# Performance work log

Measured on AMD Instinct MI355X. Metric: run time of the kernel, lower is better.

## Reference

```python
import jax, jax.numpy as jnp
import numpy as np

K = 16
REP = 128
ASZ = 6
AENC = 64
BSK = 2048 * K  # bs*K flat batch


def _lin(k, fin, fout):
    return jax.random.normal(k, (fin, fout), jnp.float32) / np.float32(np.sqrt(fin))


def setup_inputs() -> dict:
    key = jax.random.key(0)
    ks = jax.random.split(key, 20)
    inp = {
        "lambda1": jax.random.normal(ks[0], (BSK, REP), jnp.float32),
        "actions": jax.random.normal(ks[1], (BSK, ASZ), jnp.float32),
    }
    # (fan_in, hidden, fan_out) per rlkit Mlp((hidden,), out, in)
    specs = {
        "le": (REP, REP, REP),            # lambda_encoder
        "ae": (ASZ, REP, AENC),           # action_encoder
        "aef": (AENC + REP, REP, REP),    # action_effect_network
        "aat": (AENC + REP, REP, 1),      # action_attention_network
        "pe": (2 * REP, 2 * REP, REP),    # pairwise_encoder_network
        "ie": (REP, REP, AENC),           # interaction_effect_network
        "ia": (REP, REP, 1),              # interaction_attention_network
        "fm": (AENC + REP, REP, REP),     # final_merge_network
    }
    i = 2
    for name, (fin, h, fout) in specs.items():
        inp[name + "_W1"] = _lin(ks[i], fin, h)
        inp[name + "_b1"] = jnp.zeros((h,), jnp.float32)
        inp[name + "_W2"] = _lin(ks[i + 1], h, fout)
        inp[name + "_b2"] = jnp.zeros((fout,), jnp.float32)
        i += 2
    return inp


def _mlp(x, W1, b1, W2, b2, out_act):
    h = jax.nn.elu(x @ W1 + b1)
    return out_act(h @ W2 + b2)


# constant all-pairs index lists (i != j), i-major as in the torch loop
_II = np.array([i for i in range(K) for j in range(K) if i != j])
_JJ = np.array([j for i in range(K) for j in range(K) if i != j])


def reference(lambda1, actions,
              le_W1, le_b1, le_W2, le_b2,
              ae_W1, ae_b1, ae_W2, ae_b2,
              aef_W1, aef_b1, aef_W2, aef_b2,
              aat_W1, aat_b1, aat_W2, aat_b2,
              pe_W1, pe_b1, pe_W2, pe_b2,
              ie_W1, ie_b1, ie_W2, ie_b2,
              ia_W1, ia_b1, ia_W2, ia_b2,
              fm_W1, fm_b1, fm_W2, fm_b2):
    elu, sig = jax.nn.elu, jax.nn.sigmoid
    ident = lambda z: z

    enc_flat = _mlp(lambda1, le_W1, le_b1, le_W2, le_b2, elu)        # (BSK, REP)
    a_enc = _mlp(actions, ae_W1, ae_b1, ae_W2, ae_b2, elu)           # (BSK, AENC)
    la = jnp.concatenate([enc_flat, a_enc], -1)                      # (BSK, REP+AENC)
    a_eff = _mlp(la, aef_W1, aef_b1, aef_W2, aef_b2, elu)            # (BSK, REP)
    a_att = _mlp(la, aat_W1, aat_b1, aat_W2, aat_b2, sig)            # (BSK, 1)
    enc = (a_eff * a_att).reshape(-1, K, REP)                        # (bs, K, REP)
    bs = enc.shape[0]

    # all ordered pairs (i, j), i != j -> concat sender/receiver states
    all_pairs = jnp.concatenate([enc[:, _II], enc[:, _JJ]], -1)      # (bs, K*(K-1), 2*REP)
    all_pairs = all_pairs.reshape(bs * K, K - 1, 2 * REP)

    pi = _mlp(all_pairs, pe_W1, pe_b1, pe_W2, pe_b2, elu)            # (bs*K, K-1, REP)
    effect = _mlp(pi, ie_W1, ie_b1, ie_W2, ie_b2, elu)               # (bs*K, K-1, AENC)
    attention = _mlp(pi, ia_W1, ia_b1, ia_W2, ia_b2, sig)            # (bs*K, K-1, 1)
    total_effect = (effect * attention).sum(1)                       # (bs*K, AENC)

    lam_eff = jnp.concatenate([enc_flat, total_effect], -1)          # (bs*K, REP+AENC)
    new_lambdas = _mlp(lam_eff, fm_W1, fm_b1, fm_W2, fm_b2, ident)   # (bs*K, REP)
    return new_lambdas
```

## Files before the change

### kernel.cpp

```cpp
#include <hip/hip_runtime.h>
#include <hip/hip_bf16.h>

typedef unsigned short ushort_t;
typedef unsigned int uint_t;
typedef short bf16x8 __attribute__((ext_vector_type(8)));
typedef float f32x4 __attribute__((ext_vector_type(4)));

#define MFMA16(a, b, c) __builtin_amdgcn_mfma_f32_16x16x32_bf16((a), (b), (c), 0, 0, 0)

__device__ __forceinline__ ushort_t f2bf(float f) {
  uint_t u = __float_as_uint(f);
  u += 0x7fffu + ((u >> 16) & 1u);
  return (ushort_t)(u >> 16);
}
__device__ __forceinline__ float bf2f(ushort_t h) {
  return __uint_as_float(((uint_t)h) << 16);
}
__device__ __forceinline__ uint_t pack2(float lo, float hi) {
  union { __hip_bfloat162 h; uint_t u; } cv;
  cv.h = __float22bfloat162_rn(float2{lo, hi});
  return cv.u;
}
__device__ __forceinline__ uint2 pack4(f32x4 v) {
  uint2 o;
  o.x = pack2(v[0], v[1]);
  o.y = pack2(v[2], v[3]);
  return o;
}
__device__ __forceinline__ float eluf(float x) {
  float e = __expf(x) - 1.0f;
  return x > 0.0f ? x : e;
}
__device__ __forceinline__ float sigmf(float x) {
  return 1.0f / (1.0f + __expf(-x));
}
__device__ __forceinline__ int lds_off(int row, int colb, int ccb) {
  return row * ccb + (colb ^ ((row & 7) << 4));
}

constexpr size_t OFF_ENCF = 0;
constexpr size_t OFF_ENC  = 4194304;
constexpr size_t OFF_TEFF = 8388608;
constexpr size_t OFF_FR   = 10485760;

constexpr int FR_LE_W1  = 0;
constexpr int FR_LE_W2  = 16384;
constexpr int FR_AE_W2  = 32768;
constexpr int FR_AEF_W1 = 40960;
constexpr int FR_AAT_W1 = 65536;
constexpr int FR_AEF_W2 = 90112;
constexpr int FR_PE_W1  = 106496;
constexpr int FR_PE_W2  = 172032;
constexpr int FR_IE_W1  = 204800;
constexpr int FR_IE_W2  = 221184;
constexpr int FR_IA_W1  = 229376;
constexpr int FR_FM_W1  = 245760;
constexpr int FR_FM_W2  = 270336;

struct PrepDesc { const float* src; ushort_t* dst; int K; int N; };
struct PrepArgs { PrepDesc d[13]; };

__global__ __launch_bounds__(256) void prep_kernel(PrepArgs a) {
  PrepDesc p = a.d[blockIdx.y];
  int idx = blockIdx.x * 256 + threadIdx.x;
  if (idx >= p.K * p.N) return;
  int e = idx & 7;
  int lane = (idx >> 3) & 63;
  int f = idx >> 9;
  int ksteps = p.K >> 5;
  int kstep = f % ksteps;
  int ntile = f / ksteps;
  int k = kstep * 32 + ((lane >> 4) << 3) + e;
  int n = ntile * 16 + (lane & 15);
  p.dst[idx] = f2bf(p.src[k * p.N + n]);
}


template <int MT, int NT, int KS>
__device__ __forceinline__ void reg_gemm_t(const bf16x8 x[MT][KS],
                                           const ushort_t* __restrict__ wfrag,
                                           int ntile0, int lane, f32x4 acc[MT][NT]) {
  const f32x4 z = {0.f, 0.f, 0.f, 0.f};
#pragma unroll
  for (int nt = 0; nt < NT; ++nt) {
#pragma unroll
    for (int m = 0; m < MT; ++m) acc[m][nt] = z;
    const ushort_t* wf = wfrag + (size_t)((ntile0 + nt) * KS) * 512 + lane * 8;
#pragma unroll
    for (int ks = 0; ks < KS; ++ks) {
      bf16x8 wfr = *(const bf16x8*)(wf + ks * 512);
#pragma unroll
      for (int m = 0; m < MT; ++m) acc[m][nt] = MFMA16(wfr, x[m][ks], acc[m][nt]);
    }
  }
}

template <int MT, int NT, int KS>
__device__ __forceinline__ void lds_gemm_t(const ushort_t* __restrict__ Abase,
                                           const ushort_t* __restrict__ wfrag,
                                           int ntile0, int lane, f32x4 acc[MT][NT]) {
  const int r = lane & 15, q = lane >> 4;
  bf16x8 x[MT][KS];
#pragma unroll
  for (int m = 0; m < MT; ++m)
#pragma unroll
    for (int ks = 0; ks < KS; ++ks) {
      int row = m * 16 + r;
      x[m][ks] = *(const bf16x8*)((const char*)Abase + lds_off(row, ks * 64 + q * 16, KS * 64));
    }
  reg_gemm_t<MT, NT, KS>(x, wfrag, ntile0, lane, acc);
}

template <int MT, int NT, bool ELU>
__device__ __forceinline__ void add_bias_act_t(f32x4 acc[MT][NT], const float* __restrict__ bias,
                                               int col0, int lane) {
  const int q = lane >> 4;
#pragma unroll
  for (int nt = 0; nt < NT; ++nt) {
    f32x4 bv = *(const f32x4*)(bias + col0 + nt * 16 + q * 4);
#pragma unroll
    for (int m = 0; m < MT; ++m)
#pragma unroll
      for (int k = 0; k < 4; ++k) {
        float v = acc[m][nt][k] + bv[k];
        acc[m][nt][k] = ELU ? eluf(v) : v;
      }
  }
}

template <int MT, int NT, int CCB>
__device__ __forceinline__ void store_lds_t(ushort_t* Dbase, int col0, int lane,
                                            const f32x4 acc[MT][NT]) {
  const int r = lane & 15, q = lane >> 4;
#pragma unroll
  for (int m = 0; m < MT; ++m) {
    const int row = m * 16 + r;
#pragma unroll
    for (int nt = 0; nt < NT; ++nt) {
      int colb = (col0 + nt * 16 + q * 4) * 2;
      *(uint2*)((char*)Dbase + lds_off(row, colb, CCB)) = pack4(acc[m][nt]);
    }
  }
}

template <int MT, int NT>
__device__ __forceinline__ void store_global_t(ushort_t* __restrict__ G, int row0, int ncols,
                                               int col0, int lane, const f32x4 acc[MT][NT]) {
  const int r = lane & 15, q = lane >> 4;
#pragma unroll
  for (int m = 0; m < MT; ++m)
#pragma unroll
    for (int nt = 0; nt < NT; ++nt)
      *(uint2*)(G + (size_t)(row0 + m * 16 + r) * ncols + col0 + nt * 16 + q * 4) =
          pack4(acc[m][nt]);
}

__global__ __launch_bounds__(256, 2) void enc_kernel(
    const float* __restrict__ lambda1, const float* __restrict__ actions,
    const float* __restrict__ le_b1, const float* __restrict__ le_b2,
    const float* __restrict__ ae_W1, const float* __restrict__ ae_b1,
    const float* __restrict__ ae_b2, const float* __restrict__ aef_b1,
    const float* __restrict__ aef_b2, const float* __restrict__ aat_b1,
    const float* __restrict__ aat_W2, const float* __restrict__ aat_b2,
    const ushort_t* __restrict__ fr, ushort_t* __restrict__ encf, ushort_t* __restrict__ enc) {
  __shared__ ushort_t bufA[64 * 128];
  __shared__ ushort_t bufB[64 * 128];
  __shared__ ushort_t la[64 * 192];
  __shared__ float att[64];

  const int t = threadIdx.x, lane = t & 63, w = t >> 6;
  const int r = lane & 15, q = lane >> 4;
  const int rows0 = blockIdx.x * 64;

  {
    const int row = t >> 2, c0 = (t & 3) * 32;
    const float4* src = (const float4*)(lambda1 + (size_t)(rows0 + row) * 128 + c0);
#pragma unroll
    for (int j = 0; j < 8; ++j) {
      float4 v = src[j];
      f32x4 vv = {v.x, v.y, v.z, v.w};
      *(uint2*)((char*)bufA + lds_off(row, (c0 + j * 4) * 2, 256)) = pack4(vv);
    }
  }
  __syncthreads();

  f32x4 acc2[4][2];
  lds_gemm_t<4, 2, 4>(bufA, fr + FR_LE_W1, w * 2, lane, acc2);
  add_bias_act_t<4, 2, true>(acc2, le_b1, w * 32, lane);
  store_lds_t<4, 2, 256>(bufB, w * 32, lane, acc2);
  __syncthreads();
  lds_gemm_t<4, 2, 4>(bufB, fr + FR_LE_W2, w * 2, lane, acc2);
  add_bias_act_t<4, 2, true>(acc2, le_b2, w * 32, lane);
  store_lds_t<4, 2, 384>(la, w * 32, lane, acc2);
  store_global_t<4, 2>(encf, rows0, 128, w * 32, lane, acc2);
  {
    const int row = t >> 2, c0 = (t & 3) * 32;
    float a6[6];
#pragma unroll
    for (int k2 = 0; k2 < 6; ++k2) a6[k2] = actions[(size_t)(rows0 + row) * 6 + k2];
#pragma unroll
    for (int j = 0; j < 16; ++j) {
      int c = c0 + j * 2;
      float s0 = ae_b1[c], s1 = ae_b1[c + 1];
#pragma unroll
      for (int k2 = 0; k2 < 6; ++k2) {
        s0 += a6[k2] * ae_W1[k2 * 128 + c];
        s1 += a6[k2] * ae_W1[k2 * 128 + c + 1];
      }
      *(uint_t*)((char*)bufA + lds_off(row, c * 2, 256)) = pack2(eluf(s0), eluf(s1));
    }
  }
  __syncthreads();
  {
    f32x4 acc1[4][1];
    lds_gemm_t<4, 1, 4>(bufA, fr + FR_AE_W2, w, lane, acc1);
    add_bias_act_t<4, 1, true>(acc1, ae_b2, w * 16, lane);
    store_lds_t<4, 1, 384>(la, 128 + w * 16, lane, acc1);
  }
  __syncthreads();
  lds_gemm_t<4, 2, 6>(la, fr + FR_AEF_W1, w * 2, lane, acc2);
  add_bias_act_t<4, 2, true>(acc2, aef_b1, w * 32, lane);
  store_lds_t<4, 2, 256>(bufA, w * 32, lane, acc2);
  lds_gemm_t<4, 2, 6>(la, fr + FR_AAT_W1, w * 2, lane, acc2);
  add_bias_act_t<4, 2, true>(acc2, aat_b1, w * 32, lane);
  store_lds_t<4, 2, 256>(bufB, w * 32, lane, acc2);
  __syncthreads();
  lds_gemm_t<4, 2, 4>(bufA, fr + FR_AEF_W2, w * 2, lane, acc2);
  add_bias_act_t<4, 2, true>(acc2, aef_b2, w * 32, lane);
  {
    const int row = t >> 2, s = t & 3;
    float sum = 0.f;
#pragma unroll
    for (int j = 0; j < 32; ++j) {
      int c = s * 32 + j;
      sum += bf2f(*(const ushort_t*)((const char*)bufB + lds_off(row, c * 2, 256))) * aat_W2[c];
    }
    sum += __shfl_xor(sum, 1);
    sum += __shfl_xor(sum, 2);
    if (s == 0) att[row] = sigmf(sum + aat_b2[0]);
  }
  __syncthreads();
#pragma unroll
  for (int mt = 0; mt < 4; ++mt) {
    float av = att[mt * 16 + r];
#pragma unroll
    for (int nt = 0; nt < 2; ++nt) {
      f32x4 sv = acc2[mt][nt];
      sv[0] *= av; sv[1] *= av; sv[2] *= av; sv[3] *= av;
      *(uint2*)(enc + (size_t)(rows0 + mt * 16 + r) * 128 + w * 32 + nt * 16 + q * 4) = pack4(sv);
    }
  }
}

__global__ __launch_bounds__(256, 3) void pair_kernel(
    const ushort_t* __restrict__ enc, const ushort_t* __restrict__ fr,
    const float* __restrict__ pe_b1, const float* __restrict__ pe_b2,
    const float* __restrict__ ie_b1, const float* __restrict__ ie_b2,
    const float* __restrict__ ia_b1, const float* __restrict__ ia_W2,
    const float* __restrict__ ia_b2, ushort_t* __restrict__ teff) {
  __shared__ ushort_t bufH[32 * 256];
  __shared__ ushort_t bufPi[32 * 128];
  __shared__ float att[32];

  const int t = threadIdx.x, lane = t & 63, w = t >> 6;
  const int r = lane & 15, q = lane >> 4;
  const int g0 = blockIdx.x * 2;
  const int b = g0 >> 4;

  bf16x8 x[2][8];
#pragma unroll
  for (int mt = 0; mt < 2; ++mt) {
    const int im = (g0 + mt) & 15;
#pragma unroll
    for (int ks = 0; ks < 8; ++ks) {
      const int srow = (ks < 4) ? im : r;
      const int k = (ks & 3) * 32 + q * 8;
      x[mt][ks] = *(const bf16x8*)(enc + (size_t)(b * 16 + srow) * 128 + k);
    }
  }
  {
    f32x4 acc[2][4];
    reg_gemm_t<2, 4, 8>(x, fr + FR_PE_W1, w * 4, lane, acc);
    add_bias_act_t<2, 4, true>(acc, pe_b1, w * 64, lane);
    store_lds_t<2, 4, 512>(bufH, w * 64, lane, acc);
  }
  __syncthreads();
  {
    f32x4 acc[2][2];
    lds_gemm_t<2, 2, 8>(bufH, fr + FR_PE_W2, w * 2, lane, acc);
    add_bias_act_t<2, 2, true>(acc, pe_b2, w * 32, lane);
    store_lds_t<2, 2, 256>(bufPi, w * 32, lane, acc);
  }
  __syncthreads();
  {
    f32x4 acc[2][2];
    lds_gemm_t<2, 2, 4>(bufPi, fr + FR_IE_W1, w * 2, lane, acc);
    add_bias_act_t<2, 2, true>(acc, ie_b1, w * 32, lane);
    store_lds_t<2, 2, 256>(bufH, w * 32, lane, acc);
    lds_gemm_t<2, 2, 4>(bufPi, fr + FR_IA_W1, w * 2, lane, acc);
    add_bias_act_t<2, 2, true>(acc, ia_b1, w * 32, lane);
    store_lds_t<2, 2, 256>(bufH + 32 * 128, w * 32, lane, acc);
  }
  __syncthreads();
  f32x4 eff[2][1];
  lds_gemm_t<2, 1, 4>(bufH, fr + FR_IE_W2, w, lane, eff);
  add_bias_act_t<2, 1, true>(eff, ie_b2, w * 16, lane);
  {
    const int row = t >> 3, s = t & 7;
    const char* hia = (const char*)(bufH + 32 * 128);
    float sum = 0.f;
#pragma unroll
    for (int j = 0; j < 16; ++j) {
      int c = s * 16 + j;
      sum += bf2f(*(const ushort_t*)(hia + lds_off(row, c * 2, 256))) * ia_W2[c];
    }
    sum += __shfl_xor(sum, 1);
    sum += __shfl_xor(sum, 2);
    sum += __shfl_xor(sum, 4);
    if (s == 0) att[row] = sigmf(sum + ia_b2[0]);
  }
  __syncthreads();
#pragma unroll
  for (int mt = 0; mt < 2; ++mt) {
    const int im = (g0 + mt) & 15;
    const float av = (r == im) ? 0.f : att[mt * 16 + r];
    float v0 = eff[mt][0][0] * av, v1 = eff[mt][0][1] * av;
    float v2 = eff[mt][0][2] * av, v3 = eff[mt][0][3] * av;
#pragma unroll
    for (int d = 1; d < 16; d <<= 1) {
      v0 += __shfl_xor(v0, d);
      v1 += __shfl_xor(v1, d);
      v2 += __shfl_xor(v2, d);
      v3 += __shfl_xor(v3, d);
    }
    if (r == 0) {
      uint2 p;
      p.x = pack2(v0, v1);
      p.y = pack2(v2, v3);
      *(uint2*)(teff + (size_t)(g0 + mt) * 64 + w * 16 + q * 4) = p;
    }
  }
}

__global__ __launch_bounds__(256, 2) void fm_kernel(
    const ushort_t* __restrict__ encf, const ushort_t* __restrict__ teff,
    const ushort_t* __restrict__ fr, const float* __restrict__ fm_b1,
    const float* __restrict__ fm_b2, float* __restrict__ out) {
  __shared__ ushort_t bufH[64 * 128];
  const int t = threadIdx.x, lane = t & 63, w = t >> 6;
  const int r = lane & 15, q = lane >> 4;
  const int rows0 = blockIdx.x * 64;

  bf16x8 x[4][6];
#pragma unroll
  for (int mt = 0; mt < 4; ++mt) {
    const size_t row = rows0 + mt * 16 + r;
#pragma unroll
    for (int ks = 0; ks < 6; ++ks) {
      x[mt][ks] = (ks < 4) ? *(const bf16x8*)(encf + row * 128 + ks * 32 + q * 8)
                           : *(const bf16x8*)(teff + row * 64 + (ks - 4) * 32 + q * 8);
    }
  }
  f32x4 acc[4][2];
  reg_gemm_t<4, 2, 6>(x, fr + FR_FM_W1, w * 2, lane, acc);
  add_bias_act_t<4, 2, true>(acc, fm_b1, w * 32, lane);
  store_lds_t<4, 2, 256>(bufH, w * 32, lane, acc);
  __syncthreads();
  lds_gemm_t<4, 2, 4>(bufH, fr + FR_FM_W2, w * 2, lane, acc);
  add_bias_act_t<4, 2, false>(acc, fm_b2, w * 32, lane);
#pragma unroll
  for (int mt = 0; mt < 4; ++mt)
#pragma unroll
    for (int nt = 0; nt < 2; ++nt)
      *(f32x4*)(out + (size_t)(rows0 + mt * 16 + r) * 128 + w * 32 + nt * 16 + q * 4) =
          acc[mt][nt];
}

extern "C" void kernel_launch(void* const* d_in, const int* in_sizes, int n_in,
                              void* d_out, int out_size, void* d_ws, size_t ws_size,
                              hipStream_t stream) {
  (void)in_sizes; (void)n_in; (void)out_size; (void)ws_size;
  const float* lambda1 = (const float*)d_in[0];
  const float* actions = (const float*)d_in[1];

  ushort_t* ws = (ushort_t*)d_ws;
  ushort_t* encf = ws + OFF_ENCF;
  ushort_t* enc  = ws + OFF_ENC;
  ushort_t* teff = ws + OFF_TEFF;
  ushort_t* fr   = ws + OFF_FR;

  PrepArgs pa;
  const int src_idx[13] = {2, 4, 8, 10, 14, 12, 18, 20, 22, 24, 26, 30, 32};
  const int foff[13] = {FR_LE_W1, FR_LE_W2, FR_AE_W2, FR_AEF_W1, FR_AAT_W1, FR_AEF_W2,
                        FR_PE_W1, FR_PE_W2, FR_IE_W1, FR_IE_W2, FR_IA_W1, FR_FM_W1, FR_FM_W2};
  const int Ks[13] = {128, 128, 128, 192, 192, 128, 256, 256, 128, 128, 128, 192, 128};
  const int Ns[13] = {128, 128, 64, 128, 128, 128, 256, 128, 128, 64, 128, 128, 128};
  for (int i = 0; i < 13; ++i) {
    pa.d[i].src = (const float*)d_in[src_idx[i]];
    pa.d[i].dst = fr + foff[i];
    pa.d[i].K = Ks[i];
    pa.d[i].N = Ns[i];
  }
  prep_kernel<<<dim3(256, 13), 256, 0, stream>>>(pa);

  enc_kernel<<<512, 256, 0, stream>>>(
      lambda1, actions,
      (const float*)d_in[3], (const float*)d_in[5],
      (const float*)d_in[6], (const float*)d_in[7],
      (const float*)d_in[9],
      (const float*)d_in[11], (const float*)d_in[13],
      (const float*)d_in[15], (const float*)d_in[16],
      (const float*)d_in[17],
      fr, encf, enc);

  pair_kernel<<<16384, 256, 0, stream>>>(
      enc, fr,
      (const float*)d_in[19], (const float*)d_in[21],
      (const float*)d_in[23], (const float*)d_in[25],
      (const float*)d_in[27], (const float*)d_in[28],
      (const float*)d_in[29],
      teff);

  fm_kernel<<<512, 256, 0, stream>>>(encf, teff, fr,
                                     (const float*)d_in[31], (const float*)d_in[33],
                                     (float*)d_out);
}
```

Before: 409.1 us.

## Factor pairwise first layer into per-entity U/V projections computed once

The first pairwise-encoder layer W1·[enc_i; enc_j] is split into U=enc·W1_top and V=enc·W1_bottom, computed once per entity in a new uv_kernel. The pair kernel then only adds U_i+V_j+bias and applies ELU, which removes the K-fold redundant 256-wide GEMM per pair. Smaller changes go with it: the input fragments are now shared between the two GEMMs that read the same operand, the pair blocks are remapped to a new order, and occupancy is raised to 4. The trade-off is an extra kernel launch, a global round trip for U and V, and pre-activations stored in bf16 before the add, which may change rounding slightly.

Result: faster. 392.1 us (-4.2%).

```diff
diff --git a/kernel.cpp b/kernel.cpp
--- a/kernel.cpp
+++ b/kernel.cpp
@@ -42,6 +42,8 @@
 constexpr size_t OFF_ENC  = 4194304;
 constexpr size_t OFF_TEFF = 8388608;
 constexpr size_t OFF_FR   = 10485760;
+constexpr size_t OFF_U    = 10772480;
+constexpr size_t OFF_V    = 19161088;
 
 constexpr int FR_LE_W1  = 0;
 constexpr int FR_LE_W2  = 16384;
@@ -76,7 +78,7 @@
 }
 
 
-template <int MT, int NT, int KS>
+template <int MT, int NT, int KS, int KSTR = KS>
 __device__ __forceinline__ void reg_gemm_t(const bf16x8 x[MT][KS],
                                            const ushort_t* __restrict__ wfrag,
                                            int ntile0, int lane, f32x4 acc[MT][NT]) {
@@ -85,7 +87,7 @@
   for (int nt = 0; nt < NT; ++nt) {
 #pragma unroll
     for (int m = 0; m < MT; ++m) acc[m][nt] = z;
-    const ushort_t* wf = wfrag + (size_t)((ntile0 + nt) * KS) * 512 + lane * 8;
+    const ushort_t* wf = wfrag + (size_t)((ntile0 + nt) * KSTR) * 512 + lane * 8;
 #pragma unroll
     for (int ks = 0; ks < KS; ++ks) {
       bf16x8 wfr = *(const bf16x8*)(wf + ks * 512);
@@ -93,21 +95,27 @@
       for (int m = 0; m < MT; ++m) acc[m][nt] = MFMA16(wfr, x[m][ks], acc[m][nt]);
     }
   }
+}
+
+template <int MT, int KS>
+__device__ __forceinline__ void lds_load_x(const ushort_t* __restrict__ Abase, int lane,
+                                           bf16x8 x[MT][KS]) {
+  const int r = lane & 15, q = lane >> 4;
+#pragma unroll
+  for (int m = 0; m < MT; ++m)
+#pragma unroll
+    for (int ks = 0; ks < KS; ++ks) {
+      int row = m * 16 + r;
+      x[m][ks] = *(const bf16x8*)((const char*)Abase + lds_off(row, ks * 64 + q * 16, KS * 64));
+    }
 }
 
 template <int MT, int NT, int KS>
 __device__ __forceinline__ void lds_gemm_t(const ushort_t* __restrict__ Abase,
                                            const ushort_t* __restrict__ wfrag,
                                            int ntile0, int lane, f32x4 acc[MT][NT]) {
-  const int r = lane & 15, q = lane >> 4;
   bf16x8 x[MT][KS];
-#pragma unroll
-  for (int m = 0; m < MT; ++m)
-#pragma unroll
-    for (int ks = 0; ks < KS; ++ks) {
-      int row = m * 16 + r;
-      x[m][ks] = *(const bf16x8*)((const char*)Abase + lds_off(row, ks * 64 + q * 16, KS * 64));
-    }
+  lds_load_x<MT, KS>(Abase, lane, x);
   reg_gemm_t<MT, NT, KS>(x, wfrag, ntile0, lane, acc);
 }
 
@@ -163,9 +171,9 @@
     const float* __restrict__ aef_b2, const float* __restrict__ aat_b1,
     const float* __restrict__ aat_W2, const float* __restrict__ aat_b2,
     const ushort_t* __restrict__ fr, ushort_t* __restrict__ encf, ushort_t* __restrict__ enc) {
-  __shared__ ushort_t bufA[64 * 128];
-  __shared__ ushort_t bufB[64 * 128];
-  __shared__ ushort_t la[64 * 192];
+  __shared__ __align__(16) ushort_t bufA[64 * 128];
+  __shared__ __align__(16) ushort_t bufB[64 * 128];
+  __shared__ __align__(16) ushort_t la[64 * 192];
   __shared__ float att[64];
 
   const int t = threadIdx.x, lane = t & 63, w = t >> 6;
@@ -218,12 +226,16 @@
     store_lds_t<4, 1, 384>(la, 128 + w * 16, lane, acc1);
   }
   __syncthreads();
-  lds_gemm_t<4, 2, 6>(la, fr + FR_AEF_W1, w * 2, lane, acc2);
-  add_bias_act_t<4, 2, true>(acc2, aef_b1, w * 32, lane);
-  store_lds_t<4, 2, 256>(bufA, w * 32, lane, acc2);
-  lds_gemm_t<4, 2, 6>(la, fr + FR_AAT_W1, w * 2, lane, acc2);
-  add_bias_act_t<4, 2, true>(acc2, aat_b1, w * 32, lane);
-  store_lds_t<4, 2, 256>(bufB, w * 32, lane, acc2);
+  {
+    bf16x8 xla[4][6];
+    lds_load_x<4, 6>(la, lane, xla);
+    reg_gemm_t<4, 2, 6>(xla, fr + FR_AEF_W1, w * 2, lane, acc2);
+    add_bias_act_t<4, 2, true>(acc2, aef_b1, w * 32, lane);
+    store_lds_t<4, 2, 256>(bufA, w * 32, lane, acc2);
+    reg_gemm_t<4, 2, 6>(xla, fr + FR_AAT_W1, w * 2, lane, acc2);
+    add_bias_act_t<4, 2, true>(acc2, aat_b1, w * 32, lane);
+    store_lds_t<4, 2, 256>(bufB, w * 32, lane, acc2);
+  }
   __syncthreads();
   lds_gemm_t<4, 2, 4>(bufA, fr + FR_AEF_W2, w * 2, lane, acc2);
   add_bias_act_t<4, 2, true>(acc2, aef_b2, w * 32, lane);
@@ -252,62 +264,94 @@
   }
 }
 
-__global__ __launch_bounds__(256, 3) void pair_kernel(
-    const ushort_t* __restrict__ enc, const ushort_t* __restrict__ fr,
+__global__ __launch_bounds__(256, 2) void uv_kernel(const ushort_t* __restrict__ enc,
+                                                    const ushort_t* __restrict__ fr,
+                                                    ushort_t* __restrict__ U,
+                                                    ushort_t* __restrict__ V) {
+  const int t = threadIdx.x, lane = t & 63, w = t >> 6;
+  const int r = lane & 15, q = lane >> 4;
+  const int rows0 = blockIdx.x * 64;
+  const int half = blockIdx.y;
+
+  bf16x8 x[4][4];
+#pragma unroll
+  for (int m = 0; m < 4; ++m)
+#pragma unroll
+    for (int ks = 0; ks < 4; ++ks)
+      x[m][ks] = *(const bf16x8*)(enc + (size_t)(rows0 + m * 16 + r) * 128 + ks * 32 + q * 8);
+
+  f32x4 acc[4][4];
+  reg_gemm_t<4, 4, 4, 8>(x, fr + FR_PE_W1 + half * 4 * 512, w * 4, lane, acc);
+  store_global_t<4, 4>(half ? V : U, rows0, 256, w * 64, lane, acc);
+}
+
+__global__ __launch_bounds__(256, 4) void pair_kernel(
+    const ushort_t* __restrict__ U, const ushort_t* __restrict__ V,
+    const ushort_t* __restrict__ fr,
     const float* __restrict__ pe_b1, const float* __restrict__ pe_b2,
     const float* __restrict__ ie_b1, const float* __restrict__ ie_b2,
     const float* __restrict__ ia_b1, const float* __restrict__ ia_W2,
     const float* __restrict__ ia_b2, ushort_t* __restrict__ teff) {
-  __shared__ ushort_t bufH[32 * 256];
-  __shared__ ushort_t bufPi[32 * 128];
+  __shared__ __align__(16) ushort_t hid[32 * 256];
+  __shared__ __align__(16) ushort_t bufPi[32 * 128];
   __shared__ float att[32];
 
   const int t = threadIdx.x, lane = t & 63, w = t >> 6;
   const int r = lane & 15, q = lane >> 4;
-  const int g0 = blockIdx.x * 2;
+  const int orig = ((blockIdx.x & 7) << 11) + (blockIdx.x >> 3);
+  const int g0 = orig * 2;
   const int b = g0 >> 4;
 
-  bf16x8 x[2][8];
-#pragma unroll
-  for (int mt = 0; mt < 2; ++mt) {
-    const int im = (g0 + mt) & 15;
-#pragma unroll
-    for (int ks = 0; ks < 8; ++ks) {
-      const int srow = (ks < 4) ? im : r;
-      const int k = (ks & 3) * 32 + q * 8;
-      x[mt][ks] = *(const bf16x8*)(enc + (size_t)(b * 16 + srow) * 128 + k);
-    }
-  }
-  {
-    f32x4 acc[2][4];
-    reg_gemm_t<2, 4, 8>(x, fr + FR_PE_W1, w * 4, lane, acc);
-    add_bias_act_t<2, 4, true>(acc, pe_b1, w * 64, lane);
-    store_lds_t<2, 4, 512>(bufH, w * 64, lane, acc);
+  {
+    const int token = t >> 3, c0 = (t & 7) * 32;
+    const int im = (g0 + (token >> 4)) & 15;
+    const ushort_t* Ur = U + (size_t)(b * 16 + im) * 256 + c0;
+    const ushort_t* Vr = V + (size_t)(b * 16 + (token & 15)) * 256 + c0;
+    const float* bp = pe_b1 + c0;
+#pragma unroll
+    for (int j4 = 0; j4 < 4; ++j4) {
+      bf16x8 uu = *(const bf16x8*)(Ur + j4 * 8);
+      bf16x8 vv = *(const bf16x8*)(Vr + j4 * 8);
+      f32x4 b0 = *(const f32x4*)(bp + j4 * 8);
+      f32x4 b1 = *(const f32x4*)(bp + j4 * 8 + 4);
+      float h[8];
+#pragma unroll
+      for (int e = 0; e < 8; ++e) {
+        float bb = (e < 4) ? b0[e] : b1[e - 4];
+        h[e] = eluf(bf2f((ushort_t)uu[e]) + bf2f((ushort_t)vv[e]) + bb);
+      }
+      uint4 pk;
+      pk.x = pack2(h[0], h[1]); pk.y = pack2(h[2], h[3]);
+      pk.z = pack2(h[4], h[5]); pk.w = pack2(h[6], h[7]);
+      *(uint4*)((char*)hid + lds_off(token, (c0 + j4 * 8) * 2, 512)) = pk;
+    }
   }
   __syncthreads();
   {
     f32x4 acc[2][2];
-    lds_gemm_t<2, 2, 8>(bufH, fr + FR_PE_W2, w * 2, lane, acc);
+    lds_gemm_t<2, 2, 8>(hid, fr + FR_PE_W2, w * 2, lane, acc);
     add_bias_act_t<2, 2, true>(acc, pe_b2, w * 32, lane);
     store_lds_t<2, 2, 256>(bufPi, w * 32, lane, acc);
   }
   __syncthreads();
   {
+    bf16x8 x2[2][4];
+    lds_load_x<2, 4>(bufPi, lane, x2);
     f32x4 acc[2][2];
-    lds_gemm_t<2, 2, 4>(bufPi, fr + FR_IE_W1, w * 2, lane, acc);
+    reg_gemm_t<2, 2, 4>(x2, fr + FR_IE_W1, w * 2, lane, acc);
     add_bias_act_t<2, 2, true>(acc, ie_b1, w * 32, lane);
-    store_lds_t<2, 2, 256>(bufH, w * 32, lane, acc);
-    lds_gemm_t<2, 2, 4>(bufPi, fr + FR_IA_W1, w * 2, lane, acc);
+    store_lds_t<2, 2, 256>(hid, w * 32, lane, acc);
+    reg_gemm_t<2, 2, 4>(x2, fr + FR_IA_W1, w * 2, lane, acc);
     add_bias_act_t<2, 2, true>(acc, ia_b1, w * 32, lane);
-    store_lds_t<2, 2, 256>(bufH + 32 * 128, w * 32, lane, acc);
+    store_lds_t<2, 2, 256>(hid + 32 * 128, w * 32, lane, acc);
   }
   __syncthreads();
   f32x4 eff[2][1];
-  lds_gemm_t<2, 1, 4>(bufH, fr + FR_IE_W2, w, lane, eff);
+  lds_gemm_t<2, 1, 4>(hid, fr + FR_IE_W2, w, lane, eff);
   add_bias_act_t<2, 1, true>(eff, ie_b2, w * 16, lane);
   {
     const int row = t >> 3, s = t & 7;
-    const char* hia = (const char*)(bufH + 32 * 128);
+    const char* hia = (const char*)(hid + 32 * 128);
     float sum = 0.f;
 #pragma unroll
     for (int j = 0; j < 16; ++j) {
@@ -346,7 +390,7 @@
     const ushort_t* __restrict__ encf, const ushort_t* __restrict__ teff,
     const ushort_t* __restrict__ fr, const float* __restrict__ fm_b1,
     const float* __restrict__ fm_b2, float* __restrict__ out) {
-  __shared__ ushort_t bufH[64 * 128];
+  __shared__ __align__(16) ushort_t bufH[64 * 128];
   const int t = threadIdx.x, lane = t & 63, w = t >> 6;
   const int r = lane & 15, q = lane >> 4;
   const int rows0 = blockIdx.x * 64;
@@ -388,6 +432,8 @@
   ushort_t* enc  = ws + OFF_ENC;
   ushort_t* teff = ws + OFF_TEFF;
   ushort_t* fr   = ws + OFF_FR;
+  ushort_t* U    = ws + OFF_U;
+  ushort_t* V    = ws + OFF_V;
 
   PrepArgs pa;
   const int src_idx[13] = {2, 4, 8, 10, 14, 12, 18, 20, 22, 24, 26, 30, 32};
@@ -413,8 +459,10 @@
       (const float*)d_in[17],
       fr, encf, enc);
 
+  uv_kernel<<<dim3(512, 2), 256, 0, stream>>>(enc, fr, U, V);
+
   pair_kernel<<<16384, 256, 0, stream>>>(
-      enc, fr,
+      U, V, fr,
       (const float*)d_in[19], (const float*)d_in[21],
       (const float*)d_in[23], (const float*)d_in[25],
       (const float*)d_in[27], (const float*)d_in[28],
```
